# Kernel optimization log

Hardware: AMD Instinct MI355X
Metric: run time of the kernel (lower is better)

## Reference

```python
import jax, jax.numpy as jnp
import numpy as np

N_GENES_TOTAL = 2000
N_FREQ = 50
E_DIM = 10
N_FRAGMENTS = 131072
N_CELLS = 200
N_GENES_MB = 500
ENC_DIM = 4 * N_FREQ  # 200


def setup_inputs() -> dict:
    key = jax.random.key(0)
    k0, k1, k2, k3 = jax.random.split(key, 4)
    # fragment coordinates (start/end positions around the TSS, ~kb scale)
    coordinates = jax.random.normal(k0, (N_FRAGMENTS, 2), dtype=jnp.float32) * 1000.0
    # sorted ragged cell-x-gene segment index (required by segment_*_coo)
    local_cellxgene_ix = jnp.sort(
        jax.random.randint(k1, (N_FRAGMENTS,), 0, N_CELLS * N_GENES_MB)
    )
    # genes of interest in this minibatch (indices into the global gene table)
    genes_oi = jax.random.randint(k2, (N_GENES_MB,), 0, N_GENES_TOTAL)
    # consistent per-fragment gene mapping
    genemapping = genes_oi[local_cellxgene_ix % N_GENES_MB]
    # FragmentEmbedder params
    stdv = 1.0 / np.sqrt(E_DIM)
    W1 = jax.random.uniform(k3, (N_GENES_TOTAL, ENC_DIM, E_DIM), dtype=jnp.float32,
                            minval=-stdv, maxval=stdv)
    b1 = jnp.zeros((N_GENES_TOTAL, E_DIM), dtype=jnp.float32)
    # EmbeddingToExpression params, 'default' init: first 5 ones, rest zero, last -1
    w2 = np.zeros((N_GENES_TOTAL, E_DIM), dtype=np.float32)
    w2[:, :5] = 1.0
    w2[:, -1] = -1.0
    w2 = jnp.asarray(w2)
    b2 = jnp.zeros((N_GENES_TOTAL,), dtype=jnp.float32)
    return dict(coordinates=coordinates, genemapping=genemapping,
                local_cellxgene_ix=local_cellxgene_ix, genes_oi=genes_oi,
                W1=W1, b1=b1, w2=w2, b2=b2, cell_n=N_CELLS, gene_n=N_GENES_MB)


def _sine_encode(coordinates):
    nf = N_FREQ
    i = jnp.arange(1, nf + 1, dtype=coordinates.dtype)
    freqs = jnp.repeat(1.0 / (1000.0 ** (2.0 * i / nf)), 2)            # [2*nf]
    shifts = jnp.tile(jnp.array([0.0, jnp.pi / 2], coordinates.dtype), nf)  # [2*nf]
    # [F,2,1]*[2nf] -> [F,2,2nf] -> flatten last two -> [F, 4*nf]
    enc = jnp.sin((coordinates[..., None] * freqs + shifts)
                  .reshape(coordinates.shape[0], -1))
    return enc


def reference(coordinates, genemapping, local_cellxgene_ix, genes_oi,
              W1, b1, w2, b2, cell_n, gene_n):
    # FragmentEmbedder: sine encoding + per-gene linear + sigmoid
    enc = _sine_encode(coordinates)                                   # [F, 200]
    h = jnp.einsum('fe,feo->fo', enc, W1[genemapping]) + b1[genemapping]  # [F, 10]
    h = jax.nn.sigmoid(h)
    # EmbeddingGenePooler: segment-sum over sorted cellxgene index
    pooled = jax.ops.segment_sum(h, local_cellxgene_ix,
                                 num_segments=cell_n * gene_n,
                                 indices_are_sorted=True)             # [C*G, 10]
    pooled = pooled.reshape(cell_n, gene_n, -1)                       # [C, G, 10]
    # EmbeddingToExpression: per-gene weighted sum + bias
    out = (pooled * w2[genes_oi]).sum(-1) + b2[genes_oi]              # [C, G]
    return out
```

## Files before the change

kernel.cpp:

```cpp
#include <hip/hip_runtime.h>

#define NFRAG   131072
#define NCELLS  200
#define NGENES  500
#define NSEG    (NCELLS * NGENES)
#define EDIM    10
#define NFREQ   50
#define W1_ROW  2000
#define BLOCK   256
#define NWAVE   (BLOCK / 64)
#define MAXT    448

__global__ __launch_bounds__(256) void bounds_kernel(
    const int* __restrict__ cxg, int* __restrict__ off)
{
    int f = blockIdx.x * 256 + threadIdx.x;
    if (f >= NFRAG) return;
    int cur = cxg[f];
    int nxt = (f + 1 < NFRAG) ? cxg[f + 1] : NSEG;
    if (f == 0)
        for (int s = 0; s <= cur; ++s) off[s] = 0;
    for (int s = cur + 1; s <= nxt; ++s) off[s] = f + 1;
}

__global__ __launch_bounds__(BLOCK) void gene_kernel(
    const float* __restrict__ coords,
    const int*   __restrict__ off,
    const int*   __restrict__ genes_oi,
    const float* __restrict__ W1,
    const float* __restrict__ b1,
    const float* __restrict__ w2,
    const float* __restrict__ b2,
    float* __restrict__ out)
{
    __shared__ float outacc[NCELLS];
    __shared__ unsigned int flist[MAXT];
    __shared__ int wtot[NWAVE + 1];

    const int g    = blockIdx.x;
    const int t    = threadIdx.x;
    const int lane = t & 63;
    const int wid  = t >> 6;
    const int gg   = genes_oi[g];

    if (t < NCELLS) outacc[t] = 0.0f;

    int lo = 0, cnt = 0;
    if (t < NCELLS) {
        int seg = t * NGENES + g;
        lo  = off[seg];
        cnt = off[seg + 1] - lo;
    }
    int x = cnt;
    #pragma unroll
    for (int d = 1; d < 64; d <<= 1) {
        int y = __shfl_up(x, d, 64);
        if (lane >= d) x += y;
    }
    if (lane == 63) wtot[wid] = x;
    __syncthreads();
    if (t == 0) {
        int s = 0;
        #pragma unroll
        for (int w = 0; w < NWAVE; ++w) { int v = wtot[w]; wtot[w] = s; s += v; }
        wtot[NWAVE] = s;
    }
    __syncthreads();
    int base = wtot[wid] + (x - cnt);
    for (int i = 0; i < cnt; ++i)
        if (base + i < MAXT)
            flist[base + i] = ((unsigned)t << 17) | (unsigned)(lo + i);
    const int Tfull = wtot[NWAVE];
    const int T = (Tfull < MAXT) ? Tfull : MAXT;
    __syncthreads();

    const float* Wg = W1 + (size_t)gg * W1_ROW;
    float rB1[EDIM], rW2[EDIM];
    #pragma unroll
    for (int o = 0; o < EDIM; ++o) {
        rB1[o] = b1[gg * EDIM + o];
        rW2[o] = w2[gg * EDIM + o];
    }

    for (int i = t; i < T; i += BLOCK) {
        unsigned p = flist[i];
        int f = p & 0x1FFFF, c = p >> 17;
        float2 co = ((const float2*)coords)[f];

        float acc[EDIM];
        #pragma unroll
        for (int o = 0; o < EDIM; ++o) acc[o] = rB1[o];

        #pragma unroll 2
        for (int k = 0; k < NFREQ; ++k) {
            float fr = exp2f(-(float)(k + 1) * (9.965784284662087f / 25.0f));
            #pragma unroll
            for (int cc = 0; cc < 2; ++cc) {
                float xv = (cc ? co.y : co.x) * fr;
                float n = rintf(xv * 0.15915494309189535f);
                float r = fmaf(n, -6.28125f, xv);
                r = fmaf(n, -0.0019353071795864769f, r);
                float s  = __sinf(r);
                float cs = __cosf(r);
                const float4* q = (const float4*)(Wg + (cc * 100 + 2 * k) * EDIM);
                float4 q0 = q[0], q1 = q[1], q2 = q[2], q3 = q[3], q4 = q[4];
                acc[0] = fmaf(s,  q0.x, acc[0]); acc[1] = fmaf(s,  q0.y, acc[1]);
                acc[2] = fmaf(s,  q0.z, acc[2]); acc[3] = fmaf(s,  q0.w, acc[3]);
                acc[4] = fmaf(s,  q1.x, acc[4]); acc[5] = fmaf(s,  q1.y, acc[5]);
                acc[6] = fmaf(s,  q1.z, acc[6]); acc[7] = fmaf(s,  q1.w, acc[7]);
                acc[8] = fmaf(s,  q2.x, acc[8]); acc[9] = fmaf(s,  q2.y, acc[9]);
                acc[0] = fmaf(cs, q2.z, acc[0]); acc[1] = fmaf(cs, q2.w, acc[1]);
                acc[2] = fmaf(cs, q3.x, acc[2]); acc[3] = fmaf(cs, q3.y, acc[3]);
                acc[4] = fmaf(cs, q3.z, acc[4]); acc[5] = fmaf(cs, q3.w, acc[5]);
                acc[6] = fmaf(cs, q4.x, acc[6]); acc[7] = fmaf(cs, q4.y, acc[7]);
                acc[8] = fmaf(cs, q4.z, acc[8]); acc[9] = fmaf(cs, q4.w, acc[9]);
            }
        }

        float sum = 0.0f;
        #pragma unroll
        for (int o = 0; o < EDIM; ++o) {
            float h = 1.0f / (1.0f + __expf(-acc[o]));
            sum = fmaf(h, rW2[o], sum);
        }
        atomicAdd(&outacc[c], sum);
    }
    __syncthreads();

    if (t < NCELLS) out[t * NGENES + g] = outacc[t] + b2[gg];
}

extern "C" void kernel_launch(void* const* d_in, const int* in_sizes, int n_in,
                              void* d_out, int out_size, void* d_ws, size_t ws_size,
                              hipStream_t stream)
{
    const float* coords   = (const float*)d_in[0];
    const int*   cxg      = (const int*)  d_in[2];
    const int*   genes_oi = (const int*)  d_in[3];
    const float* W1       = (const float*)d_in[4];
    const float* b1       = (const float*)d_in[5];
    const float* w2       = (const float*)d_in[6];
    const float* b2       = (const float*)d_in[7];
    float* out = (float*)d_out;
    int*   off = (int*)d_ws;

    bounds_kernel<<<(NFRAG + 255) / 256, 256, 0, stream>>>(cxg, off);
    gene_kernel<<<NGENES, BLOCK, 0, stream>>>(coords, off, genes_oi,
                                              W1, b1, w2, b2, out);
}
```

Before: 114.8 us.

## Compute per-gene projection with bf16 MFMA over 16-fragment tiles per wave

Replaces the per-thread scalar FMA dot product over the 200-dim sine encoding with a wave-level bf16 16x16x32 MFMA. Each wave handles a tile of 16 fragments, and the per-gene W1 slice is preloaded into registers as bf16 B fragments. The sine/cosine encoding is now computed cooperatively across lanes instead of fully per fragment. This cuts the FMA count and the redundant W1 loads, but bf16 rounding of both the encoding and the weights adds precision risk. Output columns are padded from 10 to 16, the K dimension is padded to 224, and each row needs shuffle reductions.

```diff
diff --git a/kernel.cpp b/kernel.cpp
--- a/kernel.cpp
+++ b/kernel.cpp
@@ -10,6 +10,16 @@
 #define BLOCK   256
 #define NWAVE   (BLOCK / 64)
 #define MAXT    448
+#define KSTEPS  7
+
+typedef __attribute__((ext_vector_type(8))) short short8;
+typedef __attribute__((ext_vector_type(4))) float float4v;
+
+__device__ inline unsigned short bf16rn(float f) {
+    unsigned u = __float_as_uint(f);
+    u += 0x7fffu + ((u >> 16) & 1u);
+    return (unsigned short)(u >> 16);
+}
 
 __global__ __launch_bounds__(256) void bounds_kernel(
     const int* __restrict__ cxg, int* __restrict__ off)
@@ -41,6 +51,8 @@
     const int t    = threadIdx.x;
     const int lane = t & 63;
     const int wid  = t >> 6;
+    const int n    = lane & 15;
+    const int qb   = (lane >> 4) * 8;
     const int gg   = genes_oi[g];
 
     if (t < NCELLS) outacc[t] = 0.0f;
@@ -75,55 +87,74 @@
     __syncthreads();
 
     const float* Wg = W1 + (size_t)gg * W1_ROW;
-    float rB1[EDIM], rW2[EDIM];
+    short8 Bf[KSTEPS];
     #pragma unroll
-    for (int o = 0; o < EDIM; ++o) {
-        rB1[o] = b1[gg * EDIM + o];
-        rW2[o] = w2[gg * EDIM + o];
+    for (int ks = 0; ks < KSTEPS; ++ks) {
+        short8 bv;
+        #pragma unroll
+        for (int j = 0; j < 8; ++j) {
+            int e = qb + j + 32 * ks;
+            float w = (e < 200 && n < EDIM) ? Wg[e * EDIM + n] : 0.0f;
+            bv[j] = (short)bf16rn(w);
+        }
+        Bf[ks] = bv;
+    }
+    const float b1v = (n < EDIM) ? b1[gg * EDIM + n] : 0.0f;
+    const float w2v = (n < EDIM) ? w2[gg * EDIM + n] : 0.0f;
+
+    float fr[KSTEPS * 4];
+    #pragma unroll
+    for (int ks = 0; ks < KSTEPS; ++ks) {
+        #pragma unroll
+        for (int p = 0; p < 4; ++p) {
+            int e0 = qb + 32 * ks + 2 * p;
+            int jj = e0; if (jj >= 200) jj -= 200; if (jj >= 100) jj -= 100;
+            int kf = jj >> 1;
+            fr[ks * 4 + p] = exp2f(-(float)(kf + 1) * (9.965784284662087f / 25.0f));
+        }
     }
 
-    for (int i = t; i < T; i += BLOCK) {
-        unsigned p = flist[i];
-        int f = p & 0x1FFFF, c = p >> 17;
-        float2 co = ((const float2*)coords)[f];
+    const int tiles = (T + 15) >> 4;
+    for (int tile = wid; tile < tiles; tile += NWAVE) {
+        const int tb = tile << 4;
+        int i = tb + n;
+        if (i >= T) i = T - 1;
+        unsigned pck = flist[i];
+        float2 co = ((const float2*)coords)[pck & 0x1FFFF];
 
-        float acc[EDIM];
+        float4v acc = { b1v, b1v, b1v, b1v };
+
         #pragma unroll
-        for (int o = 0; o < EDIM; ++o) acc[o] = rB1[o];
+        for (int ks = 0; ks < KSTEPS; ++ks) {
+            short8 a;
+            #pragma unroll
+            for (int p = 0; p < 4; ++p) {
+                int e0 = qb + 32 * ks + 2 * p;
+                float xv = ((e0 >= 100) ? co.y : co.x) * fr[ks * 4 + p];
+                float nn = rintf(xv * 0.15915494309189535f);
+                float r = fmaf(nn, -6.28125f, xv);
+                r = fmaf(nn, -0.0019353071795864769f, r);
+                a[2 * p]     = (short)bf16rn(__sinf(r));
+                a[2 * p + 1] = (short)bf16rn(__cosf(r));
+            }
+            acc = __builtin_amdgcn_mfma_f32_16x16x32_bf16(a, Bf[ks], acc, 0, 0, 0);
+        }
 
-        #pragma unroll 2
-        for (int k = 0; k < NFREQ; ++k) {
-            float fr = exp2f(-(float)(k + 1) * (9.965784284662087f / 25.0f));
-            #pragma unroll
-            for (int cc = 0; cc < 2; ++cc) {
-                float xv = (cc ? co.y : co.x) * fr;
-                float n = rintf(xv * 0.15915494309189535f);
-                float r = fmaf(n, -6.28125f, xv);
-                r = fmaf(n, -0.0019353071795864769f, r);
-                float s  = __sinf(r);
-                float cs = __cosf(r);
-                const float4* q = (const float4*)(Wg + (cc * 100 + 2 * k) * EDIM);
-                float4 q0 = q[0], q1 = q[1], q2 = q[2], q3 = q[3], q4 = q[4];
-                acc[0] = fmaf(s,  q0.x, acc[0]); acc[1] = fmaf(s,  q0.y, acc[1]);
-                acc[2] = fmaf(s,  q0.z, acc[2]); acc[3] = fmaf(s,  q0.w, acc[3]);
-                acc[4] = fmaf(s,  q1.x, acc[4]); acc[5] = fmaf(s,  q1.y, acc[5]);
-                acc[6] = fmaf(s,  q1.z, acc[6]); acc[7] = fmaf(s,  q1.w, acc[7]);
-                acc[8] = fmaf(s,  q2.x, acc[8]); acc[9] = fmaf(s,  q2.y, acc[9]);
-                acc[0] = fmaf(cs, q2.z, acc[0]); acc[1] = fmaf(cs, q2.w, acc[1]);
-                acc[2] = fmaf(cs, q3.x, acc[2]); acc[3] = fmaf(cs, q3.y, acc[3]);
-                acc[4] = fmaf(cs, q3.z, acc[4]); acc[5] = fmaf(cs, q3.w, acc[5]);
-                acc[6] = fmaf(cs, q4.x, acc[6]); acc[7] = fmaf(cs, q4.y, acc[7]);
-                acc[8] = fmaf(cs, q4.z, acc[8]); acc[9] = fmaf(cs, q4.w, acc[9]);
+        #pragma unroll
+        for (int r = 0; r < 4; ++r) {
+            float h = 1.0f / (1.0f + __expf(-acc[r]));
+            float sv = h * w2v;
+            sv += __shfl_xor(sv, 1);
+            sv += __shfl_xor(sv, 2);
+            sv += __shfl_xor(sv, 4);
+            sv += __shfl_xor(sv, 8);
+            int row = (lane >> 4) * 4 + r;
+            int idx = tb + row;
+            if (n == 0 && idx < T) {
+                int cell = (int)(flist[idx] >> 17);
+                atomicAdd(&outacc[cell], sv);
             }
         }
-
-        float sum = 0.0f;
-        #pragma unroll
-        for (int o = 0; o < EDIM; ++o) {
-            float h = 1.0f / (1.0f + __expf(-acc[o]));
-            sum = fmaf(h, rW2[o], sum);
-        }
-        atomicAdd(&outacc[c], sum);
     }
     __syncthreads();
 
```

Result: faster. 102.0 us (-11.2%).
